# Kernel tuning notes

Measured on AMD Instinct MI355X. Metric: run time of the kernel, lower is better.

## Reference

```python
import jax, jax.numpy as jnp
import numpy as np

D_MODEL = 512

def setup_inputs() -> dict:
    key = jax.random.key(0)
    ks = jax.random.split(key, 8)
    B, SQ, SKV, D = 4, 2048, 4096, D_MODEL
    scale = 1.0 / np.sqrt(D)
    return {
        "x": jax.random.normal(ks[0], (B, SQ, D), dtype=jnp.float32),
        "encoder_out": jax.random.normal(ks[1], (B, SKV, D), dtype=jnp.float32),
        "wq": jax.random.normal(ks[2], (D, D), dtype=jnp.float32) * scale,
        "bq": jax.random.normal(ks[3], (D,), dtype=jnp.float32) * 0.01,
        "wk": jax.random.normal(ks[4], (D, D), dtype=jnp.float32) * scale,
        "bk": jax.random.normal(ks[5], (D,), dtype=jnp.float32) * 0.01,
        "wv": jax.random.normal(ks[6], (D, D), dtype=jnp.float32) * scale,
        "bv": jax.random.normal(ks[7], (D,), dtype=jnp.float32) * 0.01,
    }

def reference(x, encoder_out, wq, bq, wk, bk, wv, bv):
    # torch Linear: y = x @ W.T + b
    q = jnp.einsum('bsd,ed->bse', x, wq) + bq            # [B,Sq,D]
    k = jnp.einsum('btd,ed->bte', encoder_out, wk) + bk  # [B,Skv,D]
    v = jnp.einsum('btd,ed->bte', encoder_out, wv) + bv  # [B,Skv,D]
    d_k = q.shape[-1]
    scores = jnp.einsum('bse,bte->bst', q, k) / jnp.sqrt(jnp.asarray(d_k, q.dtype))
    weights = jax.nn.softmax(scores, axis=-1)            # [B,Sq,Skv]
    return jnp.einsum('bst,bte->bse', weights, v)        # [B,Sq,D]
```

## Files before the change

### kernel.cpp

```cpp
#include <hip/hip_runtime.h>
#include <hip/hip_bf16.h>


typedef __bf16 bf16;
typedef __attribute__((ext_vector_type(8))) __bf16 bf16x8;
typedef __attribute__((ext_vector_type(4))) float f32x4;

#define DM 512

__device__ __forceinline__ void gload_lds16(const bf16* g, bf16* l)
{
    __builtin_amdgcn_global_load_lds(
        (const __attribute__((address_space(1))) void*)g,
        (__attribute__((address_space(3))) void*)l, 16, 0, 0);
}

__global__ __launch_bounds__(256) void cvt_all_kernel(
    const float* __restrict__ x,   bf16* __restrict__ xb,
    const float* __restrict__ enc, bf16* __restrict__ encb,
    const float* __restrict__ wq,  bf16* __restrict__ wqb,
    const float* __restrict__ wk,  bf16* __restrict__ wkb,
    const float* __restrict__ wv,  bf16* __restrict__ wvb)
{
    int g = blockIdx.x * 256 + threadIdx.x;
    const float* src; bf16* dst;
    if (g < 524288)       { src = x;   dst = xb; }
    else if (g < 1572864) { g -= 524288;  src = enc; dst = encb; }
    else if (g < 1605632) { g -= 1572864; src = wq;  dst = wqb; }
    else if (g < 1638400) { g -= 1605632; src = wk;  dst = wkb; }
    else                  { g -= 1638400; src = wv;  dst = wvb; }
    const float4 f0 = *reinterpret_cast<const float4*>(src + (size_t)g * 8);
    const float4 f1 = *reinterpret_cast<const float4*>(src + (size_t)g * 8 + 4);
    bf16x8 v;
    v[0]=(bf16)f0.x; v[1]=(bf16)f0.y; v[2]=(bf16)f0.z; v[3]=(bf16)f0.w;
    v[4]=(bf16)f1.x; v[5]=(bf16)f1.y; v[6]=(bf16)f1.z; v[7]=(bf16)f1.w;
    *reinterpret_cast<bf16x8*>(dst + (size_t)g * 8) = v;
}

template<bool KV>
__global__ __launch_bounds__(256, 2) void proj_kernel(const bf16* __restrict__ A,
    const bf16* __restrict__ W0, const float* __restrict__ b0, bf16* __restrict__ out0,
    const bf16* __restrict__ W1, const float* __restrict__ b1, bf16* __restrict__ out1)
{
    __shared__ __align__(16) bf16 As[2][128][32];
    __shared__ __align__(16) bf16 W0s[2][128][32];
    __shared__ __align__(16) bf16 W1s[2][128][32];

    const int tid  = threadIdx.x;
    const int w    = tid >> 6, lane = tid & 63, quad = lane >> 4, l15 = lane & 15;
    const int wr   = w >> 1, wc = w & 1;
    const int n0   = blockIdx.x * 128;
    const int m0   = blockIdx.y * 128;

    const int lrow = lane >> 2;
    const int scol = ((lane & 3) ^ (lrow & 3)) * 8;
    const bf16* aSrc  = A  + (size_t)(m0 + lrow) * DM + scol;
    const bf16* wSrc0 = W0 + (size_t)(n0 + lrow) * DM + scol;
    const bf16* wSrc1 = KV ? (W1 + (size_t)(n0 + lrow) * DM + scol) : nullptr;

    auto stage = [&](int p, int kk) {
#pragma unroll
        for (int j = 0; j < 2; j++) {
            const int seg = 2 * w + j;
            gload_lds16(aSrc  + (size_t)(16 * seg) * DM + kk, &As[p][16 * seg][0]);
            gload_lds16(wSrc0 + (size_t)(16 * seg) * DM + kk, &W0s[p][16 * seg][0]);
            if constexpr (KV)
                gload_lds16(wSrc1 + (size_t)(16 * seg) * DM + kk, &W1s[p][16 * seg][0]);
        }
    };

    f32x4 acc0[4][4] = {}, acc1[4][4] = {};
    const int sx = (l15 & 3);

    stage(0, 0);
    __syncthreads();

    for (int step = 0; step < 16; step++) {
        const int p = step & 1;
        if (step < 15) stage(p ^ 1, (step + 1) * 32);

        bf16x8 af[4];
#pragma unroll
        for (int mt = 0; mt < 4; mt++)
            af[mt] = *reinterpret_cast<const bf16x8*>(
                &As[p][64*wr + 16*mt + l15][(quad ^ sx) * 8]);
#pragma unroll
        for (int nt = 0; nt < 4; nt++) {
            bf16x8 w0f = *reinterpret_cast<const bf16x8*>(
                &W0s[p][64*wc + 16*nt + l15][(quad ^ sx) * 8]);
#pragma unroll
            for (int mt = 0; mt < 4; mt++)
                acc0[mt][nt] = __builtin_amdgcn_mfma_f32_16x16x32_bf16(af[mt], w0f, acc0[mt][nt], 0, 0, 0);
            if constexpr (KV) {
                bf16x8 w1f = *reinterpret_cast<const bf16x8*>(
                    &W1s[p][64*wc + 16*nt + l15][(quad ^ sx) * 8]);
#pragma unroll
                for (int mt = 0; mt < 4; mt++)
                    acc1[mt][nt] = __builtin_amdgcn_mfma_f32_16x16x32_bf16(af[mt], w1f, acc1[mt][nt], 0, 0, 0);
            }
        }
        __syncthreads();
    }

#pragma unroll
    for (int mt = 0; mt < 4; mt++)
#pragma unroll
        for (int nt = 0; nt < 4; nt++) {
            const int coll = 64*wc + 16*nt + l15;
            const int rowl = 64*wr + 16*mt + quad*4;
            {
                const float bv = b0[n0 + coll];
                f32x4 c = acc0[mt][nt];
#pragma unroll
                for (int r = 0; r < 4; r++)
                    out0[(size_t)(m0 + rowl + r) * DM + n0 + coll] = (bf16)(c[r] + bv);
            }
            if constexpr (KV) {
                const float bv = b1[n0 + coll];
                f32x4 c = acc1[mt][nt];
                const int gr = m0 + rowl;
                const int bidx = gr >> 12, t = gr & 4095;
                const int e = n0 + coll;
                union { uint2 u; bf16 h[4]; } pk;
#pragma unroll
                for (int r = 0; r < 4; r++) pk.h[r] = (bf16)(c[r] + bv);
                *reinterpret_cast<uint2*>(out1 +
                    ((((size_t)(bidx*128 + (t >> 5)) * DM + e) << 5) + (t & 31))) = pk.u;
            }
        }
}

__global__ __launch_bounds__(512, 2) void attn_kernel(const bf16* __restrict__ Qb,
                                                      const bf16* __restrict__ Kb,
                                                      const bf16* __restrict__ Vtg,
                                                      float* __restrict__ Op,
                                                      float* __restrict__ lp)
{
    __shared__ __align__(16) bf16 Kt[2][64][512];
    __shared__ __align__(16) bf16 Ps[64][80];
    __shared__ float lred[64];

    const int tid  = threadIdx.x;
    const int w    = tid >> 6, lane = tid & 63, quad = lane >> 4, l15 = lane & 15;
    const int qb   = w >> 1;
    const int cb0  = (w & 1) * 2;

    const int id = blockIdx.x;
    const int combo = id & 7, qblk = id >> 3;
    const int b = combo & 3, z = combo >> 2;
    const int q0 = qblk * 64;
    const int NT = 32, tb = z * 2048;

    bf16x8 af[16];
    {
        const bf16* qsrc = Qb + (size_t)(b*2048 + q0 + 16*qb + l15) * DM + quad*8;
#pragma unroll
        for (int k4 = 0; k4 < 16; k4++) af[k4] = *reinterpret_cast<const bf16x8*>(qsrc + k4*32);
    }
    if (tid < 64) lred[tid] = 0.f;

    const bf16* kbase = Kb + (size_t)(b*4096 + tb) * DM;
#pragma unroll
    for (int i = 0; i < 8; i++) {
        const int row = w + 8*i;
        gload_lds16(kbase + (size_t)row * DM + ((lane ^ (row & 15)) * 8), &Kt[0][row][0]);
    }
    __syncthreads();

    f32x4 oacc[4][4] = {};
    float lsum[2][4] = {};
    const float kexp = 1.44269504088896f * 0.044194173824159216f;
    const int sxor = l15 << 4;

    for (int t = 0; t < NT; t++) {
        const int buf = t & 1;

        bf16x8 vf[4][2];
#pragma unroll
        for (int ks = 0; ks < 2; ks++) {
            const size_t tblk = (size_t)(b*128 + z*64 + t*2 + ks) * DM;
#pragma unroll
            for (int nt = 0; nt < 4; nt++)
                vf[nt][ks] = *reinterpret_cast<const bf16x8*>(
                    Vtg + ((tblk + 64*w + 16*nt + l15) << 5) + quad*8);
        }

        if (t + 1 < NT) {
            const bf16* ksrc = kbase + (size_t)(t + 1) * 64 * DM;
#pragma unroll
            for (int i = 0; i < 8; i++) {
                const int row = w + 8*i;
                gload_lds16(ksrc + (size_t)row * DM + ((lane ^ (row & 15)) * 8), &Kt[buf ^ 1][row][0]);
            }
        }

        f32x4 sacc[2] = {};
        const char* krowA = (const char*)&Kt[buf][16*cb0 + l15][0];
        const char* krowB = (const char*)&Kt[buf][16*cb0 + 16 + l15][0];
#pragma unroll
        for (int k4 = 0; k4 < 16; k4++) {
            const int off = (k4*64 + quad*16) ^ sxor;
            bf16x8 k0 = *reinterpret_cast<const bf16x8*>(krowA + off);
            bf16x8 k1 = *reinterpret_cast<const bf16x8*>(krowB + off);
            sacc[0] = __builtin_amdgcn_mfma_f32_16x16x32_bf16(af[k4], k0, sacc[0], 0, 0, 0);
            sacc[1] = __builtin_amdgcn_mfma_f32_16x16x32_bf16(af[k4], k1, sacc[1], 0, 0, 0);
        }

#pragma unroll
        for (int s = 0; s < 2; s++)
#pragma unroll
            for (int r = 0; r < 4; r++) {
                const float p = exp2f(sacc[s][r] * kexp);
                lsum[s][r] += p;
                Ps[16*qb + quad*4 + r][16*(cb0 + s) + l15] = (bf16)p;
            }

        asm volatile("s_waitcnt lgkmcnt(0)" ::: "memory");
        __builtin_amdgcn_s_barrier();
        __builtin_amdgcn_sched_barrier(0);

#pragma unroll
        for (int ks = 0; ks < 2; ks++) {
            bf16x8 ap[4];
#pragma unroll
            for (int mt = 0; mt < 4; mt++)
                ap[mt] = *reinterpret_cast<const bf16x8*>(&Ps[16*mt + l15][ks*32 + quad*8]);
#pragma unroll
            for (int nt = 0; nt < 4; nt++)
#pragma unroll
                for (int mt = 0; mt < 4; mt++)
                    oacc[mt][nt] = __builtin_amdgcn_mfma_f32_16x16x32_bf16(ap[mt], vf[nt][ks], oacc[mt][nt], 0, 0, 0);
        }
        __syncthreads();
    }

#pragma unroll
    for (int r = 0; r < 4; r++)
        atomicAdd(&lred[16*qb + quad*4 + r], lsum[0][r] + lsum[1][r]);
    __syncthreads();

    if (tid < 64) lp[(size_t)z * 8192 + b * 2048 + q0 + tid] = lred[tid];
#pragma unroll
    for (int mt = 0; mt < 4; mt++)
#pragma unroll
        for (int r = 0; r < 4; r++) {
            const int row = 16*mt + quad*4 + r;
            float* obase = Op + ((size_t)z * 8192 + b * 2048 + q0 + row) * DM;
#pragma unroll
            for (int nt = 0; nt < 4; nt++)
                obase[64*w + 16*nt + l15] = oacc[mt][nt][r];
        }
}

__global__ __launch_bounds__(256) void reduce_kernel(const float* __restrict__ Op,
                                                     const float* __restrict__ lp,
                                                     float* __restrict__ out)
{
    const int g = blockIdx.x * 256 + threadIdx.x;
    const size_t e = (size_t)g * 4;
    const int row = g >> 7;
    float4 o = *reinterpret_cast<const float4*>(Op + e);
    float4 a = *reinterpret_cast<const float4*>(Op + 4194304 + e);
    const float l = lp[row] + lp[8192 + row];
    const float linv = 1.0f / l;
    o.x = (o.x + a.x) * linv;
    o.y = (o.y + a.y) * linv;
    o.z = (o.z + a.z) * linv;
    o.w = (o.w + a.w) * linv;
    *reinterpret_cast<float4*>(out + e) = o;
}

extern "C" void kernel_launch(void* const* d_in, const int* in_sizes, int n_in,
                              void* d_out, int out_size, void* d_ws, size_t ws_size,
                              hipStream_t stream)
{
    const float* x   = (const float*)d_in[0];
    const float* enc = (const float*)d_in[1];
    const float* wq  = (const float*)d_in[2];
    const float* bq  = (const float*)d_in[3];
    const float* wk  = (const float*)d_in[4];
    const float* bk  = (const float*)d_in[5];
    const float* wv  = (const float*)d_in[6];
    const float* bv  = (const float*)d_in[7];
    float* out = (float*)d_out;

    char* ws = (char*)d_ws;
    bf16*  Qb   = (bf16*)ws;
    bf16*  Kb   = (bf16*)(ws + 8388608);
    bf16*  Vtg  = (bf16*)(ws + 25165824);
    bf16*  xb   = (bf16*)(ws + 41943040);
    bf16*  encb = (bf16*)(ws + 50331648);
    bf16*  wqb  = (bf16*)(ws + 67108864);
    bf16*  wkb  = (bf16*)(ws + 67633152);
    bf16*  wvb  = (bf16*)(ws + 68157440);
    float* Op   = (float*)(ws + 41943040);
    float* lp   = (float*)(ws + 41943040 + 2ull * 16777216);

    hipLaunchKernelGGL(cvt_all_kernel, dim3(6528), dim3(256), 0, stream,
                       x, xb, enc, encb, wq, wqb, wk, wkb, wv, wvb);

    hipLaunchKernelGGL((proj_kernel<false>), dim3(4, 64), dim3(256), 0, stream,
                       xb, wqb, bq, Qb, (const bf16*)nullptr, (const float*)nullptr, (bf16*)nullptr);
    hipLaunchKernelGGL((proj_kernel<true>),  dim3(4, 128), dim3(256), 0, stream,
                       encb, wkb, bk, Kb, wvb, bv, Vtg);

    hipLaunchKernelGGL(attn_kernel, dim3(256), dim3(512), 0, stream, Qb, Kb, Vtg, Op, lp);
    hipLaunchKernelGGL(reduce_kernel, dim3(4096), dim3(256), 0, stream, Op, lp, out);
}
```

Baseline: 232.0 us.

## Fuse fp32-to-bf16 conversion into projection GEMM and merge Q/KV launches

Removes the separate conversion kernel. The projection kernel now loads fp32 activations and weights straight into registers, converts them to bf16 and writes them into LDS with register double-buffering. The Q and K/V projections run in a single launch whose grid selects the role by block index. This drops the bf16 intermediate round-trip through global memory and two launches. In exchange, the async global-to-LDS loads become register-staged loads, which raises register pressure and reads twice the bytes per tile because the data is still fp32. Weights are re-read as fp32 by every block.

Measured after the change: 236.6 us. About the same (+1.9%).

```diff
diff --git a/kernel.cpp b/kernel.cpp
--- a/kernel.cpp
+++ b/kernel.cpp
@@ -15,32 +15,12 @@
         (__attribute__((address_space(3))) void*)l, 16, 0, 0);
 }
 
-__global__ __launch_bounds__(256) void cvt_all_kernel(
-    const float* __restrict__ x,   bf16* __restrict__ xb,
-    const float* __restrict__ enc, bf16* __restrict__ encb,
-    const float* __restrict__ wq,  bf16* __restrict__ wqb,
-    const float* __restrict__ wk,  bf16* __restrict__ wkb,
-    const float* __restrict__ wv,  bf16* __restrict__ wvb)
-{
-    int g = blockIdx.x * 256 + threadIdx.x;
-    const float* src; bf16* dst;
-    if (g < 524288)       { src = x;   dst = xb; }
-    else if (g < 1572864) { g -= 524288;  src = enc; dst = encb; }
-    else if (g < 1605632) { g -= 1572864; src = wq;  dst = wqb; }
-    else if (g < 1638400) { g -= 1605632; src = wk;  dst = wkb; }
-    else                  { g -= 1638400; src = wv;  dst = wvb; }
-    const float4 f0 = *reinterpret_cast<const float4*>(src + (size_t)g * 8);
-    const float4 f1 = *reinterpret_cast<const float4*>(src + (size_t)g * 8 + 4);
-    bf16x8 v;
-    v[0]=(bf16)f0.x; v[1]=(bf16)f0.y; v[2]=(bf16)f0.z; v[3]=(bf16)f0.w;
-    v[4]=(bf16)f1.x; v[5]=(bf16)f1.y; v[6]=(bf16)f1.z; v[7]=(bf16)f1.w;
-    *reinterpret_cast<bf16x8*>(dst + (size_t)g * 8) = v;
-}
-
-template<bool KV>
-__global__ __launch_bounds__(256, 2) void proj_kernel(const bf16* __restrict__ A,
-    const bf16* __restrict__ W0, const float* __restrict__ b0, bf16* __restrict__ out0,
-    const bf16* __restrict__ W1, const float* __restrict__ b1, bf16* __restrict__ out1)
+__global__ __launch_bounds__(256, 2) void proj_all_kernel(
+    const float* __restrict__ x,   const float* __restrict__ enc,
+    const float* __restrict__ wq,  const float* __restrict__ bq,
+    const float* __restrict__ wk,  const float* __restrict__ bk,
+    const float* __restrict__ wv,  const float* __restrict__ bv,
+    bf16* __restrict__ Qb, bf16* __restrict__ Kb, bf16* __restrict__ Vtg)
 {
     __shared__ __align__(16) bf16 As[2][128][32];
     __shared__ __align__(16) bf16 W0s[2][128][32];
@@ -50,34 +30,63 @@
     const int w    = tid >> 6, lane = tid & 63, quad = lane >> 4, l15 = lane & 15;
     const int wr   = w >> 1, wc = w & 1;
     const int n0   = blockIdx.x * 128;
-    const int m0   = blockIdx.y * 128;
-
-    const int lrow = lane >> 2;
-    const int scol = ((lane & 3) ^ (lrow & 3)) * 8;
-    const bf16* aSrc  = A  + (size_t)(m0 + lrow) * DM + scol;
-    const bf16* wSrc0 = W0 + (size_t)(n0 + lrow) * DM + scol;
-    const bf16* wSrc1 = KV ? (W1 + (size_t)(n0 + lrow) * DM + scol) : nullptr;
-
-    auto stage = [&](int p, int kk) {
+    const bool isQ = blockIdx.y < 64;
+    const int m0   = (isQ ? blockIdx.y : blockIdx.y - 64) * 128;
+
+    const float* A  = isQ ? x  : enc;
+    const float* W0 = isQ ? wq : wk;
+    const float* B0 = isQ ? bq : bk;
+
+    const int r    = lane >> 2;
+    const int cg   = lane & 3;
+    const int pcol = (cg ^ (r & 3)) * 8;
+
+    float4 ra[2][2], rw0[2][2], rw1[2][2];
+
+    auto gload = [&](int kk) {
 #pragma unroll
         for (int j = 0; j < 2; j++) {
-            const int seg = 2 * w + j;
-            gload_lds16(aSrc  + (size_t)(16 * seg) * DM + kk, &As[p][16 * seg][0]);
-            gload_lds16(wSrc0 + (size_t)(16 * seg) * DM + kk, &W0s[p][16 * seg][0]);
-            if constexpr (KV)
-                gload_lds16(wSrc1 + (size_t)(16 * seg) * DM + kk, &W1s[p][16 * seg][0]);
+            const int row = 16 * (2*w + j) + r;
+            const float* ap = A  + (size_t)(m0 + row) * DM + kk + cg*8;
+            const float* wp = W0 + (size_t)(n0 + row) * DM + kk + cg*8;
+            ra[j][0]  = *reinterpret_cast<const float4*>(ap);
+            ra[j][1]  = *reinterpret_cast<const float4*>(ap + 4);
+            rw0[j][0] = *reinterpret_cast<const float4*>(wp);
+            rw0[j][1] = *reinterpret_cast<const float4*>(wp + 4);
+            if (!isQ) {
+                const float* vp = wv + (size_t)(n0 + row) * DM + kk + cg*8;
+                rw1[j][0] = *reinterpret_cast<const float4*>(vp);
+                rw1[j][1] = *reinterpret_cast<const float4*>(vp + 4);
+            }
         }
     };
+    auto cvt8 = [](float4 a, float4 b) {
+        bf16x8 v;
+        v[0]=(bf16)a.x; v[1]=(bf16)a.y; v[2]=(bf16)a.z; v[3]=(bf16)a.w;
+        v[4]=(bf16)b.x; v[5]=(bf16)b.y; v[6]=(bf16)b.z; v[7]=(bf16)b.w;
+        return v;
+    };
+    auto lwrite = [&](int p) {
+#pragma unroll
+        for (int j = 0; j < 2; j++) {
+            const int row = 16 * (2*w + j) + r;
+            *reinterpret_cast<bf16x8*>(&As[p][row][pcol])  = cvt8(ra[j][0],  ra[j][1]);
+            *reinterpret_cast<bf16x8*>(&W0s[p][row][pcol]) = cvt8(rw0[j][0], rw0[j][1]);
+            if (!isQ)
+                *reinterpret_cast<bf16x8*>(&W1s[p][row][pcol]) = cvt8(rw1[j][0], rw1[j][1]);
+        }
+    };
 
     f32x4 acc0[4][4] = {}, acc1[4][4] = {};
-    const int sx = (l15 & 3);
-
-    stage(0, 0);
+    const int sx = l15 & 3;
+
+    gload(0);
+    lwrite(0);
     __syncthreads();
 
     for (int step = 0; step < 16; step++) {
         const int p = step & 1;
-        if (step < 15) stage(p ^ 1, (step + 1) * 32);
+        if (step < 15) gload((step + 1) * 32);
 
         bf16x8 af[4];
 #pragma unroll
@@ -91,7 +100,7 @@
 #pragma unroll
             for (int mt = 0; mt < 4; mt++)
                 acc0[mt][nt] = __builtin_amdgcn_mfma_f32_16x16x32_bf16(af[mt], w0f, acc0[mt][nt], 0, 0, 0);
-            if constexpr (KV) {
+            if (!isQ) {
                 bf16x8 w1f = *reinterpret_cast<const bf16x8*>(
                     &W1s[p][64*wc + 16*nt + l15][(quad ^ sx) * 8]);
 #pragma unroll
@@ -99,6 +108,7 @@
                     acc1[mt][nt] = __builtin_amdgcn_mfma_f32_16x16x32_bf16(af[mt], w1f, acc1[mt][nt], 0, 0, 0);
             }
         }
+        if (step < 15) lwrite(p ^ 1);
         __syncthreads();
     }
 
@@ -109,22 +119,23 @@
             const int coll = 64*wc + 16*nt + l15;
             const int rowl = 64*wr + 16*mt + quad*4;
             {
-                const float bv = b0[n0 + coll];
+                const float bvv = B0[n0 + coll];
                 f32x4 c = acc0[mt][nt];
-#pragma unroll
-                for (int r = 0; r < 4; r++)
-                    out0[(size_t)(m0 + rowl + r) * DM + n0 + coll] = (bf16)(c[r] + bv);
-            }
-            if constexpr (KV) {
-                const float bv = b1[n0 + coll];
+                bf16* out0 = isQ ? Qb : Kb;
+#pragma unroll
+                for (int rr = 0; rr < 4; rr++)
+                    out0[(size_t)(m0 + rowl + rr) * DM + n0 + coll] = (bf16)(c[rr] + bvv);
+            }
+            if (!isQ) {
+                const float bvv = bv[n0 + coll];
                 f32x4 c = acc1[mt][nt];
                 const int gr = m0 + rowl;
                 const int bidx = gr >> 12, t = gr & 4095;
                 const int e = n0 + coll;
                 union { uint2 u; bf16 h[4]; } pk;
 #pragma unroll
-                for (int r = 0; r < 4; r++) pk.h[r] = (bf16)(c[r] + bv);
-                *reinterpret_cast<uint2*>(out1 +
+                for (int rr = 0; rr < 4; rr++) pk.h[rr] = (bf16)(c[rr] + bvv);
+                *reinterpret_cast<uint2*>(Vtg +
                     ((((size_t)(bidx*128 + (t >> 5)) * DM + e) << 5) + (t & 31))) = pk.u;
             }
         }
@@ -288,21 +299,11 @@
     bf16*  Qb   = (bf16*)ws;
     bf16*  Kb   = (bf16*)(ws + 8388608);
     bf16*  Vtg  = (bf16*)(ws + 25165824);
-    bf16*  xb   = (bf16*)(ws + 41943040);
-    bf16*  encb = (bf16*)(ws + 50331648);
-    bf16*  wqb  = (bf16*)(ws + 67108864);
-    bf16*  wkb  = (bf16*)(ws + 67633152);
-    bf16*  wvb  = (bf16*)(ws + 68157440);
     float* Op   = (float*)(ws + 41943040);
     float* lp   = (float*)(ws + 41943040 + 2ull * 16777216);
 
-    hipLaunchKernelGGL(cvt_all_kernel, dim3(6528), dim3(256), 0, stream,
-                       x, xb, enc, encb, wq, wqb, wk, wkb, wv, wvb);
-
-    hipLaunchKernelGGL((proj_kernel<false>), dim3(4, 64), dim3(256), 0, stream,
-                       xb, wqb, bq, Qb, (const bf16*)nullptr, (const float*)nullptr, (bf16*)nullptr);
-    hipLaunchKernelGGL((proj_kernel<true>),  dim3(4, 128), dim3(256), 0, stream,
-                       encb, wkb, bk, Kb, wvb, bv, Vtg);
+    hipLaunchKernelGGL(proj_all_kernel, dim3(4, 192), dim3(256), 0, stream,
+                       x, enc, wq, bq, wk, bk, wv, bv, Qb, Kb, Vtg);
 
     hipLaunchKernelGGL(attn_kernel, dim3(256), dim3(512), 0, stream, Qb, Kb, Vtg, Op, lp);
     hipLaunchKernelGGL(reduce_kernel, dim3(4096), dim3(256), 0, stream, Op, lp, out);
```

## Halve attention block to four waves with larger per-wave register tiles

Applied to the files above, without the earlier changes.

The attention kernel now runs 256 threads (4 waves) per block instead of 512. Each wave computes a 32x32 score tile, reusing each K fragment across two Q row tiles, and accumulates a 64x128 output slice instead of 64x64. This raises register-level reuse of K and V fragments and cuts redundant Q fragment loads, but doubles accumulator registers (128 fp32 per lane for oacc) and halves the waves available to hide latency. With 256 blocks, occupancy on the CUs drops substantially.

After: 267.3 us. 15.2% more time.

```diff
diff --git a/kernel.cpp b/kernel.cpp
--- a/kernel.cpp
+++ b/kernel.cpp
@@ -130,7 +130,7 @@
         }
 }
 
-__global__ __launch_bounds__(512, 2) void attn_kernel(const bf16* __restrict__ Qb,
+__global__ __launch_bounds__(256, 1) void attn_kernel(const bf16* __restrict__ Qb,
                                                       const bf16* __restrict__ Kb,
                                                       const bf16* __restrict__ Vtg,
                                                       float* __restrict__ Op,
@@ -142,8 +142,8 @@
 
     const int tid  = threadIdx.x;
     const int w    = tid >> 6, lane = tid & 63, quad = lane >> 4, l15 = lane & 15;
-    const int qb   = w >> 1;
-    const int cb0  = (w & 1) * 2;
+    const int qh   = w >> 1;
+    const int kh   = w & 1;
 
     const int id = blockIdx.x;
     const int combo = id & 7, qblk = id >> 3;
@@ -151,23 +151,25 @@
     const int q0 = qblk * 64;
     const int NT = 32, tb = z * 2048;
 
-    bf16x8 af[16];
-    {
-        const bf16* qsrc = Qb + (size_t)(b*2048 + q0 + 16*qb + l15) * DM + quad*8;
-#pragma unroll
-        for (int k4 = 0; k4 < 16; k4++) af[k4] = *reinterpret_cast<const bf16x8*>(qsrc + k4*32);
+    bf16x8 af[2][16];
+#pragma unroll
+    for (int mt = 0; mt < 2; mt++) {
+        const bf16* qsrc = Qb + (size_t)(b*2048 + q0 + 32*qh + 16*mt + l15) * DM + quad*8;
+#pragma unroll
+        for (int k4 = 0; k4 < 16; k4++)
+            af[mt][k4] = *reinterpret_cast<const bf16x8*>(qsrc + k4*32);
     }
     if (tid < 64) lred[tid] = 0.f;
 
     const bf16* kbase = Kb + (size_t)(b*4096 + tb) * DM;
 #pragma unroll
-    for (int i = 0; i < 8; i++) {
-        const int row = w + 8*i;
+    for (int i = 0; i < 16; i++) {
+        const int row = w + 4*i;
         gload_lds16(kbase + (size_t)row * DM + ((lane ^ (row & 15)) * 8), &Kt[0][row][0]);
     }
     __syncthreads();
 
-    f32x4 oacc[4][4] = {};
+    f32x4 oacc[4][8] = {};
     float lsum[2][4] = {};
     const float kexp = 1.44269504088896f * 0.044194173824159216f;
     const int sxor = l15 << 4;
@@ -175,45 +177,50 @@
     for (int t = 0; t < NT; t++) {
         const int buf = t & 1;
 
-        bf16x8 vf[4][2];
+        bf16x8 vf[2][8];
 #pragma unroll
         for (int ks = 0; ks < 2; ks++) {
             const size_t tblk = (size_t)(b*128 + z*64 + t*2 + ks) * DM;
 #pragma unroll
-            for (int nt = 0; nt < 4; nt++)
-                vf[nt][ks] = *reinterpret_cast<const bf16x8*>(
-                    Vtg + ((tblk + 64*w + 16*nt + l15) << 5) + quad*8);
+            for (int nt = 0; nt < 8; nt++)
+                vf[ks][nt] = *reinterpret_cast<const bf16x8*>(
+                    Vtg + ((tblk + 128*w + 16*nt + l15) << 5) + quad*8);
         }
 
         if (t + 1 < NT) {
             const bf16* ksrc = kbase + (size_t)(t + 1) * 64 * DM;
 #pragma unroll
-            for (int i = 0; i < 8; i++) {
-                const int row = w + 8*i;
+            for (int i = 0; i < 16; i++) {
+                const int row = w + 4*i;
                 gload_lds16(ksrc + (size_t)row * DM + ((lane ^ (row & 15)) * 8), &Kt[buf ^ 1][row][0]);
             }
         }
 
-        f32x4 sacc[2] = {};
-        const char* krowA = (const char*)&Kt[buf][16*cb0 + l15][0];
-        const char* krowB = (const char*)&Kt[buf][16*cb0 + 16 + l15][0];
+        f32x4 sacc[2][2] = {};
+        const char* krow0 = (const char*)&Kt[buf][32*kh + l15][0];
+        const char* krow1 = (const char*)&Kt[buf][32*kh + 16 + l15][0];
 #pragma unroll
         for (int k4 = 0; k4 < 16; k4++) {
             const int off = (k4*64 + quad*16) ^ sxor;
-            bf16x8 k0 = *reinterpret_cast<const bf16x8*>(krowA + off);
-            bf16x8 k1 = *reinterpret_cast<const bf16x8*>(krowB + off);
-            sacc[0] = __builtin_amdgcn_mfma_f32_16x16x32_bf16(af[k4], k0, sacc[0], 0, 0, 0);
-            sacc[1] = __builtin_amdgcn_mfma_f32_16x16x32_bf16(af[k4], k1, sacc[1], 0, 0, 0);
-        }
-
-#pragma unroll
-        for (int s = 0; s < 2; s++)
-#pragma unroll
-            for (int r = 0; r < 4; r++) {
-                const float p = exp2f(sacc[s][r] * kexp);
-                lsum[s][r] += p;
-                Ps[16*qb + quad*4 + r][16*(cb0 + s) + l15] = (bf16)p;
-            }
+            bf16x8 k0 = *reinterpret_cast<const bf16x8*>(krow0 + off);
+            bf16x8 k1 = *reinterpret_cast<const bf16x8*>(krow1 + off);
+#pragma unroll
+            for (int mt = 0; mt < 2; mt++) {
+                sacc[mt][0] = __builtin_amdgcn_mfma_f32_16x16x32_bf16(af[mt][k4], k0, sacc[mt][0], 0, 0, 0);
+                sacc[mt][1] = __builtin_amdgcn_mfma_f32_16x16x32_bf16(af[mt][k4], k1, sacc[mt][1], 0, 0, 0);
+            }
+        }
+
+#pragma unroll
+        for (int mt = 0; mt < 2; mt++)
+#pragma unroll
+            for (int ni = 0; ni < 2; ni++)
+#pragma unroll
+                for (int r = 0; r < 4; r++) {
+                    const float p = exp2f(sacc[mt][ni][r] * kexp);
+                    lsum[mt][r] += p;
+                    Ps[32*qh + 16*mt + quad*4 + r][32*kh + 16*ni + l15] = (bf16)p;
+                }
 
         asm volatile("s_waitcnt lgkmcnt(0)" ::: "memory");
         __builtin_amdgcn_s_barrier();
@@ -221,22 +228,22 @@
 
 #pragma unroll
         for (int ks = 0; ks < 2; ks++) {
-            bf16x8 ap[4];
-#pragma unroll
-            for (int mt = 0; mt < 4; mt++)
-                ap[mt] = *reinterpret_cast<const bf16x8*>(&Ps[16*mt + l15][ks*32 + quad*8]);
-#pragma unroll
-            for (int nt = 0; nt < 4; nt++)
-#pragma unroll
-                for (int mt = 0; mt < 4; mt++)
-                    oacc[mt][nt] = __builtin_amdgcn_mfma_f32_16x16x32_bf16(ap[mt], vf[nt][ks], oacc[mt][nt], 0, 0, 0);
+#pragma unroll
+            for (int mt = 0; mt < 4; mt++) {
+                bf16x8 ap = *reinterpret_cast<const bf16x8*>(&Ps[16*mt + l15][ks*32 + quad*8]);
+#pragma unroll
+                for (int nt = 0; nt < 8; nt++)
+                    oacc[mt][nt] = __builtin_amdgcn_mfma_f32_16x16x32_bf16(ap, vf[ks][nt], oacc[mt][nt], 0, 0, 0);
+            }
         }
         __syncthreads();
     }
 
 #pragma unroll
-    for (int r = 0; r < 4; r++)
-        atomicAdd(&lred[16*qb + quad*4 + r], lsum[0][r] + lsum[1][r]);
+    for (int mt = 0; mt < 2; mt++)
+#pragma unroll
+        for (int r = 0; r < 4; r++)
+            atomicAdd(&lred[32*qh + 16*mt + quad*4 + r], lsum[mt][r]);
     __syncthreads();
 
     if (tid < 64) lp[(size_t)z * 8192 + b * 2048 + q0 + tid] = lred[tid];
@@ -247,8 +254,8 @@
             const int row = 16*mt + quad*4 + r;
             float* obase = Op + ((size_t)z * 8192 + b * 2048 + q0 + row) * DM;
 #pragma unroll
-            for (int nt = 0; nt < 4; nt++)
-                obase[64*w + 16*nt + l15] = oacc[mt][nt][r];
+            for (int nt = 0; nt < 8; nt++)
+                obase[128*w + 16*nt + l15] = oacc[mt][nt][r];
         }
 }
 
@@ -304,6 +311,6 @@
     hipLaunchKernelGGL((proj_kernel<true>),  dim3(4, 128), dim3(256), 0, stream,
                        encb, wkb, bk, Kb, wvb, bv, Vtg);
 
-    hipLaunchKernelGGL(attn_kernel, dim3(256), dim3(512), 0, stream, Qb, Kb, Vtg, Op, lp);
+    hipLaunchKernelGGL(attn_kernel, dim3(256), dim3(256), 0, stream, Qb, Kb, Vtg, Op, lp);
     hipLaunchKernelGGL(reduce_kernel, dim3(4096), dim3(256), 0, stream, Op, lp, out);
 }
```
